# Optimization experiments

Hardware: AMD Instinct MI355X
Metric: run time of the kernel (lower is better)

The kernel has to match this reference:

```python
import jax, jax.numpy as jnp
import numpy as np


def _build_schedule(N, M):
    """Round-robin (circle-method) tournament schedule of Givens rotations.

    Returns per-round, per-row arrays (R=N-1 rounds, each with N/2 disjoint pairs):
      partner[r, n]: row paired with n in round r (self if inactive)
      tpos[r, n]   : flat theta index for the pair (i<j: i*(N-1)-i*(i-1)/2 + j-i-1)
      sign[r, n]   : -1 for the lower-index row i, +1 for j, 0 if inactive
      active[r, n] : 1.0 if row participates in a rotation this round
    Pairs with min(i,j) >= M carry no theta and are skipped (identity).
    """
    assert N % 2 == 0, "even N assumed for the tournament schedule"
    R = N - 1
    players = list(range(N))
    partner = np.tile(np.arange(N, dtype=np.int32), (R, 1))
    tpos = np.zeros((R, N), np.int32)
    sign = np.zeros((R, N), np.float32)
    active = np.zeros((R, N), np.float32)
    for r in range(R):
        for k in range(N // 2):
            a, b = players[k], players[N - 1 - k]
            i, j = (a, b) if a < b else (b, a)
            if i >= M:
                continue
            t = i * (N - 1) - i * (i - 1) // 2 + (j - i - 1)
            partner[r, i], partner[r, j] = j, i
            tpos[r, i] = tpos[r, j] = t
            sign[r, i], sign[r, j] = -1.0, 1.0
            active[r, i] = active[r, j] = 1.0
        players = [players[0], players[-1]] + players[1:-1]
    return (jnp.asarray(partner), jnp.asarray(tpos),
            jnp.asarray(sign), jnp.asarray(active))


def _rotmat_forward(x, thetas, M=None):
    # x: [N, B]; applies the product of Givens rotations G(i,j,theta) round by round.
    N = x.shape[0]
    M = N if M is None else M
    sched = _build_schedule(N, M)

    def body(xc, rd):
        p, t, sg, ac = rd
        th = thetas[t]                       # [N]
        c = jnp.where(ac > 0, jnp.cos(th), 1.0)
        s = sg * jnp.sin(th)                 # 0 where inactive
        # row i: c*x[i] - s*x[j]; row j: s*x[i] + c*x[j]
        return c[:, None] * xc + s[:, None] * xc[p], None

    out, _ = jax.lax.scan(body, x, sched)
    return out


def setup_inputs() -> dict:
    key = jax.random.key(0)
    k1, k2 = jax.random.split(key)
    N, B = 512, 1024
    n_theta = N * (N - 1) // 2  # 130816 (M == N)
    x = jax.random.normal(k1, (N, B), dtype=jnp.float32)
    thetas = jax.random.normal(k2, (n_theta,), dtype=jnp.float32)
    return {"x": x, "thetas": thetas}


def reference(x, thetas):
    return _rotmat_forward(x, thetas)
```

## Files before the change

kernel.cpp:

```cpp
#include <hip/hip_runtime.h>


#define N_COLS      1024
#define PAIRS       256
#define CHUNK       8
#define CHUNK_BYTES (CHUNK * 2048)

typedef __attribute__((ext_vector_type(4))) float f32x4;

__global__ __launch_bounds__(256) void rotmat_setup(const float* __restrict__ thetas,
                                                    float2* __restrict__ cs) {
    const int r = blockIdx.x;
    const int k = threadIdx.x;
    int pu = (k == 0) ? 0 : ((k - 1 - r + 1022) % 511) + 1;
    int pv = ((510 - k - r + 1022) % 511) + 1;
    int i = min(pu, pv), j = max(pu, pv);
    int t = i * 511 - (i * (i - 1)) / 2 + (j - i - 1);
    float s, c;
    sincosf(thetas[t], &s, &c);
    float sp = (pu < pv) ? s : -s;
    int plane = (k >> 1) & 1, ln = k >> 2, slot = k & 1;
    cs[r * 256 + plane * 128 + ln * 2 + slot] = make_float2(c, sp);
}

__device__ __forceinline__ float dpp_shr1(float old, float src) {
    return __int_as_float(__builtin_amdgcn_update_dpp(
        __float_as_int(old), __float_as_int(src), 0x138, 0xF, 0xF, false));
}
__device__ __forceinline__ float dpp_shl1(float old, float src) {
    return __int_as_float(__builtin_amdgcn_update_dpp(
        __float_as_int(old), __float_as_int(src), 0x130, 0xF, 0xF, false));
}

__device__ __forceinline__ void glds16(const void* g, void* l) {
    __builtin_amdgcn_global_load_lds(
        (const __attribute__((address_space(1))) void*)g,
        (__attribute__((address_space(3))) void*)l, 16, 0, 0);
}

#define ROT(mi, C, S)                                   \
    {                                                   \
        float L = lo[mi], H = hi[mi];                   \
        lo[mi] = fmaf((C), L, -(S) * H);                \
        hi[mi] = fmaf((C), H, (S) * L);                 \
    }

#define SHIFT()                                                   \
    {                                                             \
        float nlo0 = dpp_shr1(lo[0], lo[3]);                      \
        float nhi3 = dpp_shl1(lo[3], hi[0]);                      \
        float nlo1 = is0 ? hi[0] : lo[0];                         \
        lo[3] = lo[2]; lo[2] = lo[1]; lo[1] = nlo1; lo[0] = nlo0; \
        hi[0] = hi[1]; hi[1] = hi[2]; hi[2] = hi[3]; hi[3] = nhi3;\
    }

#define ROUND(AA, BB)            \
    ROT(0, (AA).x, (AA).y)       \
    ROT(1, (AA).z, (AA).w)       \
    ROT(2, (BB).x, (BB).y)       \
    ROT(3, (BB).z, (BB).w)       \
    SHIFT()

#define DSR(dst, imm)                                          \
    asm volatile("ds_read_b128 %0, %1 offset:%c2"              \
                 : "=v"(dst) : "v"(lds_addr), "i"(imm))

#define WAITL(n)                                                   \
    asm volatile("s_waitcnt lgkmcnt(" #n ")" ::: "memory");        \
    __builtin_amdgcn_sched_barrier(0)

#define BODY(BOFF, NR)                                                        \
    {                                                                         \
        f32x4 a0, a1, a2, a3, a4, a5, a6, a7;                                 \
        f32x4 b0, b1, b2, b3, b4, b5, b6, b7;                                 \
        DSR(a0, (BOFF) + 0 * 2048); DSR(b0, (BOFF) + 0 * 2048 + 1024);        \
        DSR(a1, (BOFF) + 1 * 2048); DSR(b1, (BOFF) + 1 * 2048 + 1024);        \
        DSR(a2, (BOFF) + 2 * 2048); DSR(b2, (BOFF) + 2 * 2048 + 1024);        \
        DSR(a3, (BOFF) + 3 * 2048); DSR(b3, (BOFF) + 3 * 2048 + 1024);        \
        DSR(a4, (BOFF) + 4 * 2048); DSR(b4, (BOFF) + 4 * 2048 + 1024);        \
        DSR(a5, (BOFF) + 5 * 2048); DSR(b5, (BOFF) + 5 * 2048 + 1024);        \
        DSR(a6, (BOFF) + 6 * 2048); DSR(b6, (BOFF) + 6 * 2048 + 1024);        \
        DSR(a7, (BOFF) + 7 * 2048); DSR(b7, (BOFF) + 7 * 2048 + 1024);        \
        WAITL(14); ROUND(a0, b0)                                              \
        WAITL(12); ROUND(a1, b1)                                              \
        WAITL(10); ROUND(a2, b2)                                              \
        WAITL(8);  ROUND(a3, b3)                                              \
        WAITL(6);  ROUND(a4, b4)                                              \
        WAITL(4);  ROUND(a5, b5)                                              \
        WAITL(2);  ROUND(a6, b6)                                              \
        if ((NR) == 8) { WAITL(0); ROUND(a7, b7) }                            \
    }

#define STAGE(cix, bix)                                              \
    {                                                                \
        const char* g_ = gsrc + (size_t)(cix)*CHUNK_BYTES;           \
        char* l_ = lb + (bix)*CHUNK_BYTES;                           \
        _Pragma("unroll")                                            \
        for (int j = 0; j < 4; ++j)                                  \
            glds16(g_ + j * 1024, l_ + j * 1024);                    \
    }

#define WAITV(n) asm volatile("s_waitcnt vmcnt(" #n ")" ::: "memory")
#define BAR()                               \
    __builtin_amdgcn_s_barrier();           \
    __builtin_amdgcn_sched_barrier(0)

template <bool TAB>
__global__ __launch_bounds__(256, 1) void rotmat_main(const float* __restrict__ x,
                                                      const float* __restrict__ thetas,
                                                      const float2* __restrict__ cs,
                                                      float* __restrict__ out) {
    __shared__ f32x4 tab[2][CHUNK][2][64];

    const int lane = threadIdx.x & 63;
    const int wave = threadIdx.x >> 6;
    const int col  = (blockIdx.x << 2) + wave;
    const int k0   = lane << 2;
    const bool is0 = (lane == 0);

    float lo[4], hi[4];
#pragma unroll
    for (int m = 0; m < 4; ++m) {
        lo[m] = x[(k0 + m) * N_COLS + col];
        hi[m] = x[(511 - k0 - m) * N_COLS + col];
    }

    if constexpr (TAB) {
        const char* gsrc = (const char*)cs + (size_t)wave * 4096 + (size_t)lane * 16;
        char* lb = (char*)(&tab[0][0][0][0]) + wave * 4096;
        unsigned lds_addr;
        {
            auto p3 = (__attribute__((address_space(3))) char*)(&tab[0][0][0][0]);
            lds_addr = (unsigned)(size_t)p3 + (unsigned)(lane * 16);
        }

        STAGE(0, 0)
        STAGE(1, 1)
        WAITV(4);
        BAR();

        for (int t2 = 0; t2 < 31; ++t2) {
            BODY(0, 8)
            BAR();
            STAGE(2 * t2 + 2, 0)
            WAITV(4);
            BAR();
            BODY(16384, 8)
            BAR();
            STAGE(2 * t2 + 3, 1)
            WAITV(4);
            BAR();
        }
        BODY(0, 8)
        WAITV(0);
        BAR();
        BODY(16384, 7)
    } else {
        int pu[4], pv[4];
#pragma unroll
        for (int m = 0; m < 4; ++m) {
            pu[m] = (k0 + m == 0) ? 0 : (k0 + m);
            pv[m] = 511 - (k0 + m);
        }
        for (int r = 0; r < 511; ++r) {
#pragma unroll
            for (int m = 0; m < 4; ++m) {
                int i = min(pu[m], pv[m]), j = max(pu[m], pv[m]);
                int t = i * 511 - (i * (i - 1)) / 2 + (j - i - 1);
                float s, c;
                sincosf(thetas[t], &s, &c);
                float sp = (pu[m] < pv[m]) ? s : -s;
                ROT(m, c, sp)
            }
            SHIFT()
#pragma unroll
            for (int m = 0; m < 4; ++m) {
                pu[m] = (k0 + m == 0) ? 0 : ((pu[m] == 1) ? 511 : pu[m] - 1);
                pv[m] = (pv[m] == 1) ? 511 : pv[m] - 1;
            }
        }
    }

#pragma unroll
    for (int m = 0; m < 4; ++m) {
        out[(k0 + m) * N_COLS + col]       = lo[m];
        out[(511 - k0 - m) * N_COLS + col] = hi[m];
    }
}

extern "C" void kernel_launch(void* const* d_in, const int* in_sizes, int n_in,
                              void* d_out, int out_size, void* d_ws, size_t ws_size,
                              hipStream_t stream) {
    const float* x  = (const float*)d_in[0];
    const float* th = (const float*)d_in[1];
    float* out      = (float*)d_out;

    const size_t need = (size_t)512 * PAIRS * sizeof(float2);
    if (ws_size >= need) {
        float2* cs = (float2*)d_ws;
        rotmat_setup<<<511, PAIRS, 0, stream>>>(th, cs);
        rotmat_main<true><<<N_COLS / 4, 256, 0, stream>>>(x, th, cs, out);
    } else {
        rotmat_main<false><<<N_COLS / 4, 256, 0, stream>>>(x, th, nullptr, out);
    }
}
```

Before: 50.50 us.

## Fuse pairs of rotation rounds into precomputed 4-term combined step coefficients

A setup kernel now merges each pair of consecutive tournament rounds, together with the row shift between them, into per-element 4-coefficient linear combinations. The main kernel applies one fused step per two rounds using DPP neighbour exchanges and 4-term dot products. The final odd round is handled separately from a small table. This halves the number of dependent rotate/shift steps on the critical path. In exchange it doubles the coefficient table bandwidth through LDS, adds extra DPP ops per step, and needs an extra setup launch.

```diff
diff --git a/kernel.cpp b/kernel.cpp
--- a/kernel.cpp
+++ b/kernel.cpp
@@ -1,26 +1,65 @@
 #include <hip/hip_runtime.h>
 
 
-#define N_COLS      1024
-#define PAIRS       256
-#define CHUNK       8
-#define CHUNK_BYTES (CHUNK * 2048)
+#define N_COLS   1024
+#define PAIRS    256
 
 typedef __attribute__((ext_vector_type(4))) float f32x4;
 
-__global__ __launch_bounds__(256) void rotmat_setup(const float* __restrict__ thetas,
-                                                    float2* __restrict__ cs) {
-    const int r = blockIdx.x;
-    const int k = threadIdx.x;
+__device__ __forceinline__ float2 cs_of(const float* __restrict__ th, int r, int k) {
     int pu = (k == 0) ? 0 : ((k - 1 - r + 1022) % 511) + 1;
     int pv = ((510 - k - r + 1022) % 511) + 1;
     int i = min(pu, pv), j = max(pu, pv);
     int t = i * 511 - (i * (i - 1)) / 2 + (j - i - 1);
     float s, c;
-    sincosf(thetas[t], &s, &c);
-    float sp = (pu < pv) ? s : -s;
-    int plane = (k >> 1) & 1, ln = k >> 2, slot = k & 1;
-    cs[r * 256 + plane * 128 + ln * 2 + slot] = make_float2(c, sp);
+    sincosf(th[t], &s, &c);
+    return make_float2(c, (pu < pv) ? s : -s);
+}
+
+__global__ __launch_bounds__(256) void setup_steps(const float* __restrict__ thetas,
+                                                   float4* __restrict__ out4) {
+    const int b = blockIdx.x;
+    const int k = threadIdx.x;
+    const int r = 2 * b, rp = 2 * b + 1;
+
+    float4 L, H;
+    if (k == 0) {
+        float2 c0 = cs_of(thetas, r, 0), c1 = cs_of(thetas, r, 1), C0 = cs_of(thetas, rp, 0);
+        L = make_float4(C0.x * c0.x, -C0.x * c0.y, -C0.y * c1.y, -C0.y * c1.x);
+    } else if (k == 1) {
+        float2 c0 = cs_of(thetas, r, 0), c1 = cs_of(thetas, r, 1), C0 = cs_of(thetas, rp, 0);
+        L = make_float4(C0.y * c0.x, -C0.y * c0.y, C0.x * c1.y, C0.x * c1.x);
+    } else if (k == 2) {
+        float2 c0 = cs_of(thetas, r, 0), c2 = cs_of(thetas, r, 2), C1 = cs_of(thetas, rp, 1);
+        L = make_float4(C1.x * c0.y, C1.x * c0.x, -C1.y * c2.y, -C1.y * c2.x);
+    } else {
+        float2 ca = cs_of(thetas, r, k - 2), cb = cs_of(thetas, r, k), Cp = cs_of(thetas, rp, k - 1);
+        L = make_float4(Cp.x * ca.x, -Cp.x * ca.y, -Cp.y * cb.y, -Cp.y * cb.x);
+    }
+    if (k == 0) {
+        float2 cb = cs_of(thetas, r, 0), cc = cs_of(thetas, r, 2), Cq = cs_of(thetas, rp, 1);
+        H = make_float4(Cq.y * cb.y, Cq.y * cb.x, Cq.x * cc.y, Cq.x * cc.x);
+    } else if (k <= 253) {
+        float2 cb = cs_of(thetas, r, k), cc = cs_of(thetas, r, k + 2), Cq = cs_of(thetas, rp, k + 1);
+        H = make_float4(Cq.y * cb.x, -Cq.y * cb.y, Cq.x * cc.y, Cq.x * cc.x);
+    } else if (k == 254) {
+        float2 cb = cs_of(thetas, r, 254), cc = cs_of(thetas, r, 255), Cq = cs_of(thetas, rp, 255);
+        H = make_float4(Cq.y * cb.x, -Cq.y * cb.y, Cq.x * cc.x, -Cq.x * cc.y);
+    } else {
+        float2 ca = cs_of(thetas, r, 254), cb = cs_of(thetas, r, 255), Cq = cs_of(thetas, rp, 255);
+        H = make_float4(-Cq.y * cb.x, Cq.y * cb.y, Cq.x * ca.x, -Cq.x * ca.y);
+    }
+    const int l = k >> 2, m = k & 3;
+    out4[b * 512 + m * 64 + l]       = L;
+    out4[b * 512 + (4 + m) * 64 + l] = H;
+}
+
+__global__ __launch_bounds__(256) void setup_last(const float* __restrict__ thetas,
+                                                  float2* __restrict__ cs) {
+    const int k = threadIdx.x;
+    float2 v = cs_of(thetas, 510, k);
+    int plane = (k >> 1) & 1, l = k >> 2, slot = k & 1;
+    cs[262144 + plane * 128 + l * 2 + slot] = v;
 }
 
 __device__ __forceinline__ float dpp_shr1(float old, float src) {
@@ -40,9 +79,9 @@
 
 #define ROT(mi, C, S)                                   \
     {                                                   \
-        float L = lo[mi], H = hi[mi];                   \
-        lo[mi] = fmaf((C), L, -(S) * H);                \
-        hi[mi] = fmaf((C), H, (S) * L);                 \
+        float L_ = lo[mi], H_ = hi[mi];                 \
+        lo[mi] = fmaf((C), L_, -(S) * H_);              \
+        hi[mi] = fmaf((C), H_, (S) * L_);               \
     }
 
 #define SHIFT()                                                   \
@@ -54,12 +93,29 @@
         hi[0] = hi[1]; hi[1] = hi[2]; hi[2] = hi[3]; hi[3] = nhi3;\
     }
 
-#define ROUND(AA, BB)            \
-    ROT(0, (AA).x, (AA).y)       \
-    ROT(1, (AA).z, (AA).w)       \
-    ROT(2, (BB).x, (BB).y)       \
-    ROT(3, (BB).z, (BB).w)       \
-    SHIFT()
+#define STEP(QL0, QL1, QL2, QL3, QH0, QH1, QH2, QH3)                          \
+    {                                                                         \
+        float loH2 = dpp_shr1(lo[0], lo[2]);                                  \
+        float loH3 = dpp_shr1(lo[0], lo[3]);                                  \
+        float hiH2 = dpp_shr1(hi[0], hi[2]);                                  \
+        float hiH3 = dpp_shr1(hi[0], hi[3]);                                  \
+        float loL0 = dpp_shl1(lo[3], lo[0]);                                  \
+        float loL1 = dpp_shl1(lo[2], lo[1]);                                  \
+        float hiL0 = dpp_shl1(hi[3], hi[0]);                                  \
+        float hiL1 = dpp_shl1(hi[2], hi[1]);                                  \
+        float Cs = is0 ? lo[1] : lo[0];                                       \
+        float Ds = is0 ? hi[1] : hi[0];                                       \
+        float nl0 = (QL0).x * loH2  + (QL0).y * hiH2  + (QL0).z * Cs    + (QL0).w * Ds;    \
+        float nl1 = (QL1).x * loH3  + (QL1).y * hiH3  + (QL1).z * lo[1] + (QL1).w * hi[1]; \
+        float nl2 = (QL2).x * lo[0] + (QL2).y * hi[0] + (QL2).z * lo[2] + (QL2).w * hi[2]; \
+        float nl3 = (QL3).x * lo[1] + (QL3).y * hi[1] + (QL3).z * lo[3] + (QL3).w * hi[3]; \
+        float nh0 = (QH0).x * lo[0] + (QH0).y * hi[0] + (QH0).z * lo[2] + (QH0).w * hi[2]; \
+        float nh1 = (QH1).x * lo[1] + (QH1).y * hi[1] + (QH1).z * lo[3] + (QH1).w * hi[3]; \
+        float nh2 = (QH2).x * lo[2] + (QH2).y * hi[2] + (QH2).z * loL0  + (QH2).w * hiL0;  \
+        float nh3 = (QH3).x * lo[3] + (QH3).y * hi[3] + (QH3).z * loL1  + (QH3).w * hiL1;  \
+        lo[0] = nl0; lo[1] = nl1; lo[2] = nl2; lo[3] = nl3;                   \
+        hi[0] = nh0; hi[1] = nh1; hi[2] = nh2; hi[3] = nh3;                   \
+    }
 
 #define DSR(dst, imm)                                          \
     asm volatile("ds_read_b128 %0, %1 offset:%c2"              \
@@ -69,34 +125,50 @@
     asm volatile("s_waitcnt lgkmcnt(" #n ")" ::: "memory");        \
     __builtin_amdgcn_sched_barrier(0)
 
-#define BODY(BOFF, NR)                                                        \
+#define DS8(BOFF, st, s)                                                      \
+    DSR(P##s##0, (BOFF) + (st)*8192 + 0 * 1024);                              \
+    DSR(P##s##1, (BOFF) + (st)*8192 + 1 * 1024);                              \
+    DSR(P##s##2, (BOFF) + (st)*8192 + 2 * 1024);                              \
+    DSR(P##s##3, (BOFF) + (st)*8192 + 3 * 1024);                              \
+    DSR(P##s##4, (BOFF) + (st)*8192 + 4 * 1024);                              \
+    DSR(P##s##5, (BOFF) + (st)*8192 + 5 * 1024);                              \
+    DSR(P##s##6, (BOFF) + (st)*8192 + 6 * 1024);                              \
+    DSR(P##s##7, (BOFF) + (st)*8192 + 7 * 1024);
+
+#define STEPS(s) STEP(P##s##0, P##s##1, P##s##2, P##s##3, P##s##4, P##s##5, P##s##6, P##s##7)
+
+#define CBODY_FULL(BOFF)                                                      \
     {                                                                         \
-        f32x4 a0, a1, a2, a3, a4, a5, a6, a7;                                 \
-        f32x4 b0, b1, b2, b3, b4, b5, b6, b7;                                 \
-        DSR(a0, (BOFF) + 0 * 2048); DSR(b0, (BOFF) + 0 * 2048 + 1024);        \
-        DSR(a1, (BOFF) + 1 * 2048); DSR(b1, (BOFF) + 1 * 2048 + 1024);        \
-        DSR(a2, (BOFF) + 2 * 2048); DSR(b2, (BOFF) + 2 * 2048 + 1024);        \
-        DSR(a3, (BOFF) + 3 * 2048); DSR(b3, (BOFF) + 3 * 2048 + 1024);        \
-        DSR(a4, (BOFF) + 4 * 2048); DSR(b4, (BOFF) + 4 * 2048 + 1024);        \
-        DSR(a5, (BOFF) + 5 * 2048); DSR(b5, (BOFF) + 5 * 2048 + 1024);        \
-        DSR(a6, (BOFF) + 6 * 2048); DSR(b6, (BOFF) + 6 * 2048 + 1024);        \
-        DSR(a7, (BOFF) + 7 * 2048); DSR(b7, (BOFF) + 7 * 2048 + 1024);        \
-        WAITL(14); ROUND(a0, b0)                                              \
-        WAITL(12); ROUND(a1, b1)                                              \
-        WAITL(10); ROUND(a2, b2)                                              \
-        WAITL(8);  ROUND(a3, b3)                                              \
-        WAITL(6);  ROUND(a4, b4)                                              \
-        WAITL(4);  ROUND(a5, b5)                                              \
-        WAITL(2);  ROUND(a6, b6)                                              \
-        if ((NR) == 8) { WAITL(0); ROUND(a7, b7) }                            \
+        f32x4 Pa0, Pa1, Pa2, Pa3, Pa4, Pa5, Pa6, Pa7;                         \
+        f32x4 Pb0, Pb1, Pb2, Pb3, Pb4, Pb5, Pb6, Pb7;                         \
+        DS8(BOFF, 0, a)                                                       \
+        DS8(BOFF, 1, b)                                                       \
+        WAITL(8);  STEPS(a)                                                   \
+        DS8(BOFF, 2, a)                                                       \
+        WAITL(8);  STEPS(b)                                                   \
+        DS8(BOFF, 3, b)                                                       \
+        WAITL(8);  STEPS(a)                                                   \
+        WAITL(0);  STEPS(b)                                                   \
+    }
+
+#define CBODY_TAIL(BOFF)                                                      \
+    {                                                                         \
+        f32x4 Pa0, Pa1, Pa2, Pa3, Pa4, Pa5, Pa6, Pa7;                         \
+        f32x4 Pb0, Pb1, Pb2, Pb3, Pb4, Pb5, Pb6, Pb7;                         \
+        DS8(BOFF, 0, a)                                                       \
+        DS8(BOFF, 1, b)                                                       \
+        WAITL(8);  STEPS(a)                                                   \
+        DS8(BOFF, 2, a)                                                       \
+        WAITL(8);  STEPS(b)                                                   \
+        WAITL(0);  STEPS(a)                                                   \
     }
 
 #define STAGE(cix, bix)                                              \
     {                                                                \
-        const char* g_ = gsrc + (size_t)(cix)*CHUNK_BYTES;           \
-        char* l_ = lb + (bix)*CHUNK_BYTES;                           \
+        const char* g_ = gsrc + (size_t)(cix)*32768;                 \
+        char* l_ = lb + (bix)*32768;                                 \
         _Pragma("unroll")                                            \
-        for (int j = 0; j < 4; ++j)                                  \
+        for (int j = 0; j < 8; ++j)                                  \
             glds16(g_ + j * 1024, l_ + j * 1024);                    \
     }
 
@@ -110,7 +182,7 @@
                                                       const float* __restrict__ thetas,
                                                       const float2* __restrict__ cs,
                                                       float* __restrict__ out) {
-    __shared__ f32x4 tab[2][CHUNK][2][64];
+    __shared__ f32x4 tab[2][4][8][64];
 
     const int lane = threadIdx.x & 63;
     const int wave = threadIdx.x >> 6;
@@ -126,8 +198,12 @@
     }
 
     if constexpr (TAB) {
-        const char* gsrc = (const char*)cs + (size_t)wave * 4096 + (size_t)lane * 16;
-        char* lb = (char*)(&tab[0][0][0][0]) + wave * 4096;
+        const float4* T4g = reinterpret_cast<const float4*>(cs);
+        float4 cL0 = T4g[131072 + lane];
+        float4 cL1 = T4g[131072 + 64 + lane];
+
+        const char* gsrc = (const char*)cs + (size_t)wave * 8192 + (size_t)lane * 16;
+        char* lb = (char*)(&tab[0][0][0][0]) + wave * 8192;
         unsigned lds_addr;
         {
             auto p3 = (__attribute__((address_space(3))) char*)(&tab[0][0][0][0]);
@@ -136,25 +212,31 @@
 
         STAGE(0, 0)
         STAGE(1, 1)
-        WAITV(4);
+        WAITV(8);
         BAR();
 
         for (int t2 = 0; t2 < 31; ++t2) {
-            BODY(0, 8)
+            CBODY_FULL(0)
             BAR();
             STAGE(2 * t2 + 2, 0)
-            WAITV(4);
-            BAR();
-            BODY(16384, 8)
+            WAITV(8);
+            BAR();
+            CBODY_FULL(32768)
             BAR();
             STAGE(2 * t2 + 3, 1)
-            WAITV(4);
-            BAR();
-        }
-        BODY(0, 8)
+            WAITV(8);
+            BAR();
+        }
+        CBODY_FULL(0)
         WAITV(0);
         BAR();
-        BODY(16384, 7)
+        CBODY_TAIL(32768)
+
+        ROT(0, cL0.x, cL0.y)
+        ROT(1, cL0.z, cL0.w)
+        ROT(2, cL1.x, cL1.y)
+        ROT(3, cL1.z, cL1.w)
+        SHIFT()
     } else {
         int pu[4], pv[4];
 #pragma unroll
@@ -195,11 +277,12 @@
     const float* th = (const float*)d_in[1];
     float* out      = (float*)d_out;
 
-    const size_t need = (size_t)512 * PAIRS * sizeof(float2);
+    const size_t need = (size_t)256 * 8192 + 2048;
     if (ws_size >= need) {
-        float2* cs = (float2*)d_ws;
-        rotmat_setup<<<511, PAIRS, 0, stream>>>(th, cs);
-        rotmat_main<true><<<N_COLS / 4, 256, 0, stream>>>(x, th, cs, out);
+        float4* t4 = (float4*)d_ws;
+        setup_steps<<<255, 256, 0, stream>>>(th, t4);
+        setup_last<<<1, 256, 0, stream>>>(th, (float2*)d_ws);
+        rotmat_main<true><<<N_COLS / 4, 256, 0, stream>>>(x, th, (const float2*)d_ws, out);
     } else {
         rotmat_main<false><<<N_COLS / 4, 256, 0, stream>>>(x, th, nullptr, out);
     }
```

After: 85.38 us. 1.69x slower.
